# Performance work log

Hardware: AMD Instinct MI355X
Metric: run time of the kernel (lower is better)

The kernel has to match this reference:

```python
import jax, jax.numpy as jnp
import numpy as np

N, F_IN, E = 50000, 128, 800000
D1, D2, D3, NUM_LAYERS = 90, 80, 50, 4
EPS = 1e-5


def _gcn_norm(edge_index, n):
    # add self-loops, compute symmetric normalization deg^{-1/2} A_hat deg^{-1/2}
    loops = jnp.arange(n, dtype=edge_index.dtype)
    src = jnp.concatenate([edge_index[0], loops])
    dst = jnp.concatenate([edge_index[1], loops])
    deg = jax.ops.segment_sum(jnp.ones_like(src, dtype=jnp.float32), dst, num_segments=n)
    deg_isqrt = jnp.where(deg > 0, jax.lax.rsqrt(deg), 0.0)
    norm = deg_isqrt[src] * deg_isqrt[dst]  # [E+N]
    return src, dst, norm


def _gcn_conv(x, w, b, src, dst, norm, n):
    h = x @ w                                   # [N, d_out] dense transform first
    msg = h[src] * norm[:, None]                # gather + scale  [E+N, d_out]
    out = jax.ops.segment_sum(msg, dst, num_segments=n)  # scatter-add
    return out + b


def _bn(x, gamma, beta):
    # batch-statistics BatchNorm1d over node dim
    mu = jnp.mean(x, axis=0)
    var = jnp.var(x, axis=0)
    return (x - mu) * jax.lax.rsqrt(var + EPS) * gamma + beta


def setup_inputs() -> dict:
    key = jax.random.key(0)
    ks = jax.random.split(key, 16)
    s = lambda *sh: 1.0 / np.sqrt(sh[0])
    inp = {
        'x': jax.random.normal(ks[0], (N, F_IN), jnp.float32),
        'edge_index': jax.random.randint(ks[1], (2, E), 0, N, dtype=jnp.int32),
        'conv1_w': jax.random.normal(ks[2], (F_IN, D1), jnp.float32) * s(F_IN),
        'conv1_b': jnp.zeros((D1,), jnp.float32),
        'convs_w': jax.random.normal(ks[3], (NUM_LAYERS - 1, D1, D1), jnp.float32) * s(D1),
        'convs_b': jnp.zeros((NUM_LAYERS - 1, D1), jnp.float32),
        'bn1_g': jnp.ones((D1,), jnp.float32), 'bn1_b': jnp.zeros((D1,), jnp.float32),
        'fc1_w': jax.random.normal(ks[4], (D1, D2), jnp.float32) * s(D1),
        'fc1_b': jnp.zeros((D2,), jnp.float32),
        'bn2_g': jnp.ones((D2,), jnp.float32), 'bn2_b': jnp.zeros((D2,), jnp.float32),
        'fc2_w': jax.random.normal(ks[5], (D2, D3), jnp.float32) * s(D2),
        'fc2_b': jnp.zeros((D3,), jnp.float32),
        'bn3_g': jnp.ones((D3,), jnp.float32), 'bn3_b': jnp.zeros((D3,), jnp.float32),
        'fc3_w': jax.random.normal(ks[6], (D3, 1), jnp.float32) * s(D3),
        'fc3_b': jnp.zeros((1,), jnp.float32),
    }
    return inp


def reference(x, edge_index, conv1_w, conv1_b, convs_w, convs_b,
              bn1_g, bn1_b, fc1_w, fc1_b, bn2_g, bn2_b,
              fc2_w, fc2_b, bn3_g, bn3_b, fc3_w, fc3_b):
    n = x.shape[0]
    src, dst, norm = _gcn_norm(edge_index, n)
    h = jax.nn.relu(_gcn_conv(x, conv1_w, conv1_b, src, dst, norm, n))
    for i in range(convs_w.shape[0]):
        h = jax.nn.relu(_gcn_conv(h, convs_w[i], convs_b[i], src, dst, norm, n))
        h = _bn(h, bn1_g, bn1_b)
        # dropout is identity in eval mode
    h = jax.nn.relu(_bn(h @ fc1_w + fc1_b, bn2_g, bn2_b))
    h = jax.nn.relu(_bn(h @ fc2_w + fc2_b, bn3_g, bn3_b))
    return h @ fc3_w + fc3_b
```

## Files before the change

kernel.cpp:

```cpp
#include <hip/hip_runtime.h>

#define NBLK(n, b) (((n) + (b) - 1) / (b))

#define FS 96
#define FS4 24

typedef _Float16 half8_t __attribute__((ext_vector_type(8)));
typedef float float8_t __attribute__((ext_vector_type(8)));
typedef float f32x4_t __attribute__((ext_vector_type(4)));


__global__ void count_k(const int* __restrict__ dst, int* __restrict__ cnt, int e) {
  int i = blockIdx.x * blockDim.x + threadIdx.x;
  if (i < e) atomicAdd(&cnt[dst[i]], 1);
}

__global__ void isq_k(const int* __restrict__ cnt, float* __restrict__ isq, int n) {
  int i = blockIdx.x * blockDim.x + threadIdx.x;
  if (i < n) isq[i] = rsqrtf((float)cnt[i] + 1.0f);
}

__global__ __launch_bounds__(256) void scan1_k(const int* __restrict__ cnt,
                                               int* __restrict__ rowptr,
                                               int* __restrict__ partials, int n) {
  __shared__ int ls[256];
  const int t = threadIdx.x;
  const int base = blockIdx.x * 1024 + t * 4;
  int v0 = 0, v1 = 0, v2 = 0, v3 = 0;
  if (base + 3 < n) {
    int4 q = *reinterpret_cast<const int4*>(cnt + base);
    v0 = q.x; v1 = q.y; v2 = q.z; v3 = q.w;
  } else {
    if (base < n) v0 = cnt[base];
    if (base + 1 < n) v1 = cnt[base + 1];
    if (base + 2 < n) v2 = cnt[base + 2];
  }
  int s = v0 + v1 + v2 + v3;
  ls[t] = s;
  __syncthreads();
  for (int off = 1; off < 256; off <<= 1) {
    int u = (t >= off) ? ls[t - off] : 0;
    __syncthreads();
    ls[t] += u;
    __syncthreads();
  }
  int p = ls[t] - s;
  if (t == 255) partials[blockIdx.x] = ls[255];
  if (base < n) rowptr[base] = p;
  p += v0;
  if (base + 1 < n) rowptr[base + 1] = p;
  p += v1;
  if (base + 2 < n) rowptr[base + 2] = p;
  p += v2;
  if (base + 3 < n) rowptr[base + 3] = p;
}

__global__ __launch_bounds__(256) void scan2_k(const int* __restrict__ partials,
                                               int* __restrict__ offsets, int B) {
  __shared__ int ls[256];
  const int t = threadIdx.x;
  int v = (t < B) ? partials[t] : 0;
  ls[t] = v;
  __syncthreads();
  for (int off = 1; off < 256; off <<= 1) {
    int u = (t >= off) ? ls[t - off] : 0;
    __syncthreads();
    ls[t] += u;
    __syncthreads();
  }
  if (t < B) offsets[t] = ls[t] - v;
  if (t == B - 1) offsets[B] = ls[t];
}

__global__ __launch_bounds__(256) void scan3_k(int* __restrict__ rowptr,
                                               int* __restrict__ cursor,
                                               const int* __restrict__ offsets,
                                               int n, int B) {
  const int t = threadIdx.x;
  const int base = blockIdx.x * 1024 + t * 4;
  const int off = offsets[blockIdx.x];
  if (base + 3 < n) {
    int4 q = *reinterpret_cast<const int4*>(rowptr + base);
    q.x += off; q.y += off; q.z += off; q.w += off;
    *reinterpret_cast<int4*>(rowptr + base) = q;
    *reinterpret_cast<int4*>(cursor + base) = q;
  } else {
    for (int i = base; i < n; ++i) {
      int v = rowptr[i] + off;
      rowptr[i] = v;
      cursor[i] = v;
    }
  }
  if (base == 0 && blockIdx.x == 0) rowptr[n] = offsets[B];
}

__global__ __launch_bounds__(256) void fill_part_k(
    const int* __restrict__ src, const int* __restrict__ dst,
    int* __restrict__ cursor, unsigned short* __restrict__ csr, int e, int n) {
  const int p = blockIdx.x & 7;
  const int q = blockIdx.x >> 3;
  const int nb = gridDim.x >> 3;
  const int ps = (n + 7) >> 3;
  const int lo = p * ps;
  const int hi = min(lo + ps, n);
  const int stride = nb * 256;
  for (int i = q * 256 + threadIdx.x; i < e; i += stride) {
    const int d = dst[i];
    if (d >= lo && d < hi) {
      const int pos = atomicAdd(&cursor[d], 1);
      csr[pos] = (unsigned short)src[i];
    }
  }
}


template <int K, int KP, int M, int INS, int OUTS, int XF, int EPI, int NT>
__global__ __launch_bounds__(256, 2) void gemm4_k(
    const float* __restrict__ X, const float* __restrict__ W,
    const float* __restrict__ bias, const float* __restrict__ isq,
    const float* __restrict__ scale, const float* __restrict__ shift,
    void* __restrict__ OUT, int n) {
  constexpr int KG = KP / 8;
  __shared__ _Float16 Wh[NT * KG * 16 * 8];
  const int t = threadIdx.x;
  const int tbase = blockIdx.y * NT;
  for (int idx = t; idx < KP * NT * 16; idx += 256) {
    const int k = idx / (NT * 16), cl = idx - k * (NT * 16);
    const int c = tbase * 16 + cl;
    const float v = (k < K && c < M) ? W[k * M + c] : 0.0f;
    const int tt = cl >> 4, cc = cl & 15;
    Wh[((tt * KG + (k >> 3)) * 16 + cc) * 8 + (k & 7)] = (_Float16)v;
  }
  __syncthreads();
  const int wid = t >> 6;
  const int lane = t & 63;
  const int lr = lane & 15;
  const int hk = lane >> 4;
  const int r0 = blockIdx.x * 64 + wid * 16;
  const int arow = min(r0 + lr, n - 1);
  const float* __restrict__ xp = X + (size_t)arow * INS;
  const half8_t* __restrict__ Whv = reinterpret_cast<const half8_t*>(Wh);
  f32x4_t acc[NT];
#pragma unroll
  for (int tt = 0; tt < NT; ++tt) acc[tt] = (f32x4_t){0.0f, 0.0f, 0.0f, 0.0f};
  for (int ks = 0; ks < KP; ks += 32) {
    const int kb = ks + hk * 8;
    float a[8];
    {
      float4 v0 = *reinterpret_cast<const float4*>(xp + kb);
      float4 v1 = *reinterpret_cast<const float4*>(xp + kb + 4);
      a[0] = v0.x; a[1] = v0.y; a[2] = v0.z; a[3] = v0.w;
      a[4] = v1.x; a[5] = v1.y; a[6] = v1.z; a[7] = v1.w;
    }
    if constexpr (XF == 1) {
#pragma unroll
      for (int i = 0; i < 8; ++i) a[i] = fmaxf(a[i], 0.0f);
    } else if constexpr (XF == 2 || XF == 3) {
      float4 s0 = *reinterpret_cast<const float4*>(scale + kb);
      float4 s1 = *reinterpret_cast<const float4*>(scale + kb + 4);
      float4 h0 = *reinterpret_cast<const float4*>(shift + kb);
      float4 h1 = *reinterpret_cast<const float4*>(shift + kb + 4);
      const float sc[8] = {s0.x, s0.y, s0.z, s0.w, s1.x, s1.y, s1.z, s1.w};
      const float sh[8] = {h0.x, h0.y, h0.z, h0.w, h1.x, h1.y, h1.z, h1.w};
#pragma unroll
      for (int i = 0; i < 8; ++i) {
        if constexpr (XF == 2) a[i] = fmaxf(a[i], 0.0f) * sc[i] + sh[i];
        else a[i] = fmaxf(a[i] * sc[i] + sh[i], 0.0f);
      }
    }
    half8_t af;
#pragma unroll
    for (int i = 0; i < 8; ++i) af[i] = (_Float16)a[i];
    const int kg = kb >> 3;
#pragma unroll
    for (int tt = 0; tt < NT; ++tt) {
      half8_t bf = Whv[(tt * KG + kg) * 16 + lr];
      acc[tt] = __builtin_amdgcn_mfma_f32_16x16x32_f16(af, bf, acc[tt], 0, 0, 0);
    }
  }
  const int rg = r0 + (hk << 2);
  if constexpr (EPI == 0) {
    float siq[4];
#pragma unroll
    for (int j = 0; j < 4; ++j) siq[j] = (rg + j < n) ? isq[rg + j] : 0.0f;
    _Float16* Hh = (_Float16*)OUT;
#pragma unroll
    for (int tt = 0; tt < NT; ++tt) {
      const int c = (tbase + tt) * 16 + lr;
      const int tb = c / 48;
      const int so = c % 48;
#pragma unroll
      for (int j = 0; j < 4; ++j) {
        const int row = rg + j;
        if (row < n)
          Hh[(size_t)tb * n * 48 + (size_t)row * 48 + so] =
              (_Float16)(acc[tt][j] * siq[j]);
      }
    }
  } else {
    float* O = (float*)OUT;
#pragma unroll
    for (int tt = 0; tt < NT; ++tt) {
      const int c = (tbase + tt) * 16 + lr;
      const float bv = (c < M) ? bias[c] : 0.0f;
#pragma unroll
      for (int j = 0; j < 4; ++j) {
        const int row = rg + j;
        if (row < n) O[(size_t)row * OUTS + c] = acc[tt][j] + bv;
      }
    }
  }
}


template <int K, int KP, int M, int MH, int INS, int OUTS, int XF, int EPI>
__global__ __launch_bounds__(256, 2) void gemm2_k(
    const float* __restrict__ X, const float* __restrict__ W,
    const float* __restrict__ bias, const float* __restrict__ isq,
    const float* __restrict__ scale, const float* __restrict__ shift,
    void* __restrict__ OUT, int n) {
  __shared__ float Ws[KP * MH];
  __shared__ float Sc[(XF >= 2) ? KP : 1];
  __shared__ float Sh[(XF >= 2) ? KP : 1];
  const int ms = blockIdx.y;
  for (int idx = threadIdx.x; idx < KP * MH; idx += 256) {
    int k = idx / MH;
    int m = idx - k * MH;
    int col = ms * MH + m;
    Ws[idx] = (k < K && col < M) ? W[k * M + col] : 0.0f;
  }
  if constexpr (XF >= 2) {
    for (int k = threadIdx.x; k < KP; k += 256) {
      Sc[k] = (k < K) ? scale[k] : 0.0f;
      Sh[k] = (k < K) ? shift[k] : 0.0f;
    }
  }
  __syncthreads();
  const int row = blockIdx.x * 256 + threadIdx.x;
  const bool valid = row < n;
  const float* xp = X + (size_t)(valid ? row : 0) * INS;
  float acc[MH];
#pragma unroll
  for (int m = 0; m < MH; ++m) acc[m] = 0.0f;
  for (int k0 = 0; k0 < KP; k0 += 4) {
    float4 tt = *reinterpret_cast<const float4*>(xp + k0);
    float xv[4] = {tt.x, tt.y, tt.z, tt.w};
#pragma unroll
    for (int j = 0; j < 4; ++j) {
      float xval = xv[j];
      if constexpr (XF == 1) xval = fmaxf(xval, 0.0f);
      if constexpr (XF == 2) xval = fmaxf(xval, 0.0f) * Sc[k0 + j] + Sh[k0 + j];
      if constexpr (XF == 3) xval = fmaxf(xval * Sc[k0 + j] + Sh[k0 + j], 0.0f);
      const float* wrow = &Ws[(k0 + j) * MH];
#pragma unroll
      for (int m = 0; m < MH; ++m) acc[m] += xval * wrow[m];
    }
  }
  if (!valid) return;
  float* O = (float*)OUT;
  const size_t base = (size_t)row * OUTS + ms * MH;
#pragma unroll
  for (int m = 0; m < MH; ++m) O[base + m] = acc[m] + bias[ms * MH + m];
}


__global__ __launch_bounds__(256, 6) void gather_k(
    const _Float16* __restrict__ H, const int* __restrict__ rowptr,
    const unsigned short* __restrict__ csr, const float* __restrict__ isq,
    const float* __restrict__ bias, float* __restrict__ A, int n) {
  const int wid = threadIdx.x >> 6;
  const int lane = threadIdx.x & 63;
  const int d = blockIdx.x * 4 + wid;
  if (d >= n) return;
  const int g = lane >> 4;
  const int s = lane & 15;
  const int beg = rowptr[d];
  const int end = rowptr[d + 1];
  const half8_t* __restrict__ Hp = reinterpret_cast<const half8_t*>(H);
  const int sl = (s < 6) ? s : (s - 6);
  const half8_t* __restrict__ lanebase = Hp + ((s < 6) ? 0 : (size_t)n * 6) + sl;
  float8_t acc = {0, 0, 0, 0, 0, 0, 0, 0};
  float8_t acc2 = {0, 0, 0, 0, 0, 0, 0, 0};
  if (lane < 12)
    acc += __builtin_convertvector(lanebase[(size_t)d * 6], float8_t);
  int r = beg + g;
  for (; r + 4 < end; r += 8) {
    const int v0 = (int)csr[r];
    const int v1 = (int)csr[r + 4];
    if (s < 12) {
      acc += __builtin_convertvector(lanebase[(size_t)v0 * 6], float8_t);
      acc2 += __builtin_convertvector(lanebase[(size_t)v1 * 6], float8_t);
    }
  }
  for (; r < end; r += 4) {
    const int v = (int)csr[r];
    if (s < 12) acc += __builtin_convertvector(lanebase[(size_t)v * 6], float8_t);
  }
  acc += acc2;
#pragma unroll
  for (int i = 0; i < 8; ++i) acc[i] += __shfl_xor(acc[i], 16);
#pragma unroll
  for (int i = 0; i < 8; ++i) acc[i] += __shfl_xor(acc[i], 32);
  if (lane < 12) {
    const float sc = isq[d];
    const int c = lane * 8;
    float o[8];
#pragma unroll
    for (int i = 0; i < 8; ++i)
      o[i] = acc[i] * sc + ((c + i < 90) ? bias[c + i] : 0.0f);
    float4* Ap = reinterpret_cast<float4*>(A + (size_t)d * FS + c);
    Ap[0] = make_float4(o[0], o[1], o[2], o[3]);
    Ap[1] = make_float4(o[4], o[5], o[6], o[7]);
  }
}


template <int M, bool RELU>
__global__ __launch_bounds__(256) void bn_stats4_k(const float* __restrict__ X,
                                                   float* __restrict__ gsum,
                                                   float* __restrict__ gsq, int n) {
  __shared__ float ssum[FS];
  __shared__ float ssq[FS];
  for (int i = threadIdx.x; i < FS; i += 256) { ssum[i] = 0.0f; ssq[i] = 0.0f; }
  __syncthreads();
  const int t = threadIdx.x;
  const int cq = t % FS4;
  const int rl = t / FS4;
  constexpr int ROWS = 256 / FS4;
  const float4* __restrict__ Xp = reinterpret_cast<const float4*>(X);
  if (rl < ROWS) {
    float s0 = 0, s1 = 0, s2 = 0, s3 = 0, q0 = 0, q1 = 0, q2 = 0, q3 = 0;
    for (int r = blockIdx.x * ROWS + rl; r < n; r += gridDim.x * ROWS) {
      float4 v = Xp[(size_t)r * FS4 + cq];
      if (RELU) {
        v.x = fmaxf(v.x, 0.0f); v.y = fmaxf(v.y, 0.0f);
        v.z = fmaxf(v.z, 0.0f); v.w = fmaxf(v.w, 0.0f);
      }
      s0 += v.x; q0 += v.x * v.x;
      s1 += v.y; q1 += v.y * v.y;
      s2 += v.z; q2 += v.z * v.z;
      s3 += v.w; q3 += v.w * v.w;
    }
    const int c = cq * 4;
    if (c + 0 < M) { atomicAdd(&ssum[c + 0], s0); atomicAdd(&ssq[c + 0], q0); }
    if (c + 1 < M) { atomicAdd(&ssum[c + 1], s1); atomicAdd(&ssq[c + 1], q1); }
    if (c + 2 < M) { atomicAdd(&ssum[c + 2], s2); atomicAdd(&ssq[c + 2], q2); }
    if (c + 3 < M) { atomicAdd(&ssum[c + 3], s3); atomicAdd(&ssq[c + 3], q3); }
  }
  __syncthreads();
  for (int i = threadIdx.x; i < M; i += 256) {
    atomicAdd(&gsum[i], ssum[i]);
    atomicAdd(&gsq[i], ssq[i]);
  }
}


template <int M>
__global__ void bn_final_k(const float* __restrict__ gsum, const float* __restrict__ gsq,
                           const float* __restrict__ g, const float* __restrict__ b,
                           float* __restrict__ scale, float* __restrict__ shift, float invn) {
  int c = threadIdx.x;
  if (c >= FS) return;
  if (c >= M) { scale[c] = 0.0f; shift[c] = 0.0f; return; }
  float mu = gsum[c] * invn;
  float var = gsq[c] * invn - mu * mu;
  float r = rsqrtf(var + 1e-5f);
  float sc = g[c] * r;
  scale[c] = sc;
  shift[c] = b[c] - mu * sc;
}


extern "C" void kernel_launch(void* const* d_in, const int* in_sizes, int n_in,
                              void* d_out, int out_size, void* d_ws, size_t ws_size,
                              hipStream_t stream) {
  const float* x = (const float*)d_in[0];
  const int* ei = (const int*)d_in[1];
  const float* conv1_w = (const float*)d_in[2];
  const float* conv1_b = (const float*)d_in[3];
  const float* convs_w = (const float*)d_in[4];
  const float* convs_b = (const float*)d_in[5];
  const float* bn1_g = (const float*)d_in[6];
  const float* bn1_b = (const float*)d_in[7];
  const float* fc1_w = (const float*)d_in[8];
  const float* fc1_b = (const float*)d_in[9];
  const float* bn2_g = (const float*)d_in[10];
  const float* bn2_b = (const float*)d_in[11];
  const float* fc2_w = (const float*)d_in[12];
  const float* fc2_b = (const float*)d_in[13];
  const float* bn3_g = (const float*)d_in[14];
  const float* bn3_b = (const float*)d_in[15];
  const float* fc3_w = (const float*)d_in[16];
  const float* fc3_b = (const float*)d_in[17];

  const int N = in_sizes[0] / 128;
  const int E = in_sizes[1] / 2;
  const int* src = ei;
  const int* dst = ei + E;
  const int B = NBLK(N, 1024);

  float* ws = (float*)d_ws;
  float* isq = ws;
  int* rowptr = (int*)(ws + 50048);
  int* cursor = rowptr + 50048;
  int* cnt = cursor + 50048;
  unsigned short* csr16 = (unsigned short*)(cnt + 50048);
  int* partials = (int*)(csr16 + 800000);
  int* offsets = partials + 64;
  float* stats = (float*)(offsets + 128);
  float* scale = stats + 5 * 192;
  float* shift = scale + 96;
  float* bufH = shift + 96;
  float* bufA = bufH + (size_t)N * FS;
  _Float16* bufHh = (_Float16*)bufH;

  float* gs0 = stats + 0 * 192; float* gq0 = gs0 + 96;
  float* gs1 = stats + 1 * 192; float* gq1 = gs1 + 96;
  float* gs2 = stats + 2 * 192; float* gq2 = gs2 + 96;
  float* gs3 = stats + 3 * 192; float* gq3 = gs3 + 96;
  float* gs4 = stats + 4 * 192; float* gq4 = gs4 + 96;

  hipMemsetAsync(cnt, 0, 50048 * sizeof(int), stream);
  hipMemsetAsync(stats, 0, 5 * 192 * sizeof(float), stream);
  count_k<<<NBLK(E, 256), 256, 0, stream>>>(dst, cnt, E);
  isq_k<<<NBLK(N, 256), 256, 0, stream>>>(cnt, isq, N);
  scan1_k<<<B, 256, 0, stream>>>(cnt, rowptr, partials, N);
  scan2_k<<<1, 256, 0, stream>>>(partials, offsets, B);
  scan3_k<<<B, 256, 0, stream>>>(rowptr, cursor, offsets, N, B);
  fill_part_k<<<1024, 256, 0, stream>>>(src, dst, cursor, csr16, E, N);

  const int grows = NBLK(N, 256);
  const int gmf = NBLK(N, 64);
  const int ggath = NBLK(N, 4);
  const float invn = 1.0f / (float)N;

  gemm4_k<128, 128, 90, 128, FS, 0, 0, 3><<<dim3(gmf, 2), 256, 0, stream>>>(
      x, conv1_w, nullptr, isq, nullptr, nullptr, bufHh, N);
  gather_k<<<ggath, 256, 0, stream>>>(bufHh, rowptr, csr16, isq, conv1_b, bufA, N);

  gemm4_k<90, 96, 90, FS, FS, 1, 0, 3><<<dim3(gmf, 2), 256, 0, stream>>>(
      bufA, convs_w, nullptr, isq, nullptr, nullptr, bufHh, N);
  gather_k<<<ggath, 256, 0, stream>>>(bufHh, rowptr, csr16, isq, convs_b, bufA, N);
  bn_stats4_k<90, true><<<512, 256, 0, stream>>>(bufA, gs0, gq0, N);
  bn_final_k<90><<<1, 128, 0, stream>>>(gs0, gq0, bn1_g, bn1_b, scale, shift, invn);

  gemm4_k<90, 96, 90, FS, FS, 2, 0, 3><<<dim3(gmf, 2), 256, 0, stream>>>(
      bufA, convs_w + 90 * 90, nullptr, isq, scale, shift, bufHh, N);
  gather_k<<<ggath, 256, 0, stream>>>(bufHh, rowptr, csr16, isq, convs_b + 90, bufA, N);
  bn_stats4_k<90, true><<<512, 256, 0, stream>>>(bufA, gs1, gq1, N);
  bn_final_k<90><<<1, 128, 0, stream>>>(gs1, gq1, bn1_g, bn1_b, scale, shift, invn);

  gemm4_k<90, 96, 90, FS, FS, 2, 0, 3><<<dim3(gmf, 2), 256, 0, stream>>>(
      bufA, convs_w + 2 * 90 * 90, nullptr, isq, scale, shift, bufHh, N);
  gather_k<<<ggath, 256, 0, stream>>>(bufHh, rowptr, csr16, isq, convs_b + 2 * 90, bufA, N);
  bn_stats4_k<90, true><<<512, 256, 0, stream>>>(bufA, gs2, gq2, N);
  bn_final_k<90><<<1, 128, 0, stream>>>(gs2, gq2, bn1_g, bn1_b, scale, shift, invn);

  gemm4_k<90, 96, 80, FS, FS, 2, 1, 3><<<dim3(gmf, 2), 256, 0, stream>>>(
      bufA, fc1_w, fc1_b, nullptr, scale, shift, bufH, N);
  bn_stats4_k<80, false><<<512, 256, 0, stream>>>(bufH, gs3, gq3, N);
  bn_final_k<80><<<1, 128, 0, stream>>>(gs3, gq3, bn2_g, bn2_b, scale, shift, invn);

  gemm2_k<80, 80, 50, 25, FS, FS, 3, 1><<<dim3(grows, 2), 256, 0, stream>>>(
      bufH, fc2_w, fc2_b, nullptr, scale, shift, bufA, N);
  bn_stats4_k<50, false><<<512, 256, 0, stream>>>(bufA, gs4, gq4, N);
  bn_final_k<50><<<1, 128, 0, stream>>>(gs4, gq4, bn3_g, bn3_b, scale, shift, invn);

  gemm2_k<50, 52, 1, 1, FS, 1, 3, 1><<<dim3(grows, 1), 256, 0, stream>>>(
      bufA, fc3_w, fc3_b, nullptr, scale, shift, (float*)d_out, N);
}
```

Measured before the change: 476.1 us.

## Store fp16 H row-contiguous and split GEMM columns unevenly (64+32)

```diff
diff --git a/kernel.cpp b/kernel.cpp
--- a/kernel.cpp
+++ b/kernel.cpp
@@ -114,19 +114,23 @@
 }
 
 
-template <int K, int KP, int M, int INS, int OUTS, int XF, int EPI, int NT>
+template <int K, int KP, int M, int INS, int OUTS, int XF, int EPI>
 __global__ __launch_bounds__(256, 2) void gemm4_k(
     const float* __restrict__ X, const float* __restrict__ W,
     const float* __restrict__ bias, const float* __restrict__ isq,
     const float* __restrict__ scale, const float* __restrict__ shift,
     void* __restrict__ OUT, int n) {
   constexpr int KG = KP / 8;
-  __shared__ _Float16 Wh[NT * KG * 16 * 8];
+  __shared__ _Float16 Wh[4 * KG * 16 * 8];
   const int t = threadIdx.x;
-  const int tbase = blockIdx.y * NT;
-  for (int idx = t; idx < KP * NT * 16; idx += 256) {
-    const int k = idx / (NT * 16), cl = idx - k * (NT * 16);
-    const int c = tbase * 16 + cl;
+  const int ybl = blockIdx.y;
+  const int ntiles = ybl ? 2 : 4;
+  const int tbase = ybl ? 4 : 0;
+  const int nt16 = ntiles << 4;
+  const int sh = ybl ? 5 : 6;
+  for (int idx = t; idx < KP * nt16; idx += 256) {
+    const int k = idx >> sh, cl = idx & (nt16 - 1);
+    const int c = (tbase << 4) + cl;
     const float v = (k < K && c < M) ? W[k * M + c] : 0.0f;
     const int tt = cl >> 4, cc = cl & 15;
     Wh[((tt * KG + (k >> 3)) * 16 + cc) * 8 + (k & 7)] = (_Float16)v;
@@ -140,9 +144,9 @@
   const int arow = min(r0 + lr, n - 1);
   const float* __restrict__ xp = X + (size_t)arow * INS;
   const half8_t* __restrict__ Whv = reinterpret_cast<const half8_t*>(Wh);
-  f32x4_t acc[NT];
-#pragma unroll
-  for (int tt = 0; tt < NT; ++tt) acc[tt] = (f32x4_t){0.0f, 0.0f, 0.0f, 0.0f};
+  f32x4_t acc[4];
+#pragma unroll
+  for (int tt = 0; tt < 4; ++tt) acc[tt] = (f32x4_t){0.0f, 0.0f, 0.0f, 0.0f};
   for (int ks = 0; ks < KP; ks += 32) {
     const int kb = ks + hk * 8;
     float a[8];
@@ -161,11 +165,11 @@
       float4 h0 = *reinterpret_cast<const float4*>(shift + kb);
       float4 h1 = *reinterpret_cast<const float4*>(shift + kb + 4);
       const float sc[8] = {s0.x, s0.y, s0.z, s0.w, s1.x, s1.y, s1.z, s1.w};
-      const float sh[8] = {h0.x, h0.y, h0.z, h0.w, h1.x, h1.y, h1.z, h1.w};
+      const float shf[8] = {h0.x, h0.y, h0.z, h0.w, h1.x, h1.y, h1.z, h1.w};
 #pragma unroll
       for (int i = 0; i < 8; ++i) {
-        if constexpr (XF == 2) a[i] = fmaxf(a[i], 0.0f) * sc[i] + sh[i];
-        else a[i] = fmaxf(a[i] * sc[i] + sh[i], 0.0f);
+        if constexpr (XF == 2) a[i] = fmaxf(a[i], 0.0f) * sc[i] + shf[i];
+        else a[i] = fmaxf(a[i] * sc[i] + shf[i], 0.0f);
       }
     }
     half8_t af;
@@ -173,9 +177,11 @@
     for (int i = 0; i < 8; ++i) af[i] = (_Float16)a[i];
     const int kg = kb >> 3;
 #pragma unroll
-    for (int tt = 0; tt < NT; ++tt) {
-      half8_t bf = Whv[(tt * KG + kg) * 16 + lr];
-      acc[tt] = __builtin_amdgcn_mfma_f32_16x16x32_f16(af, bf, acc[tt], 0, 0, 0);
+    for (int tt = 0; tt < 4; ++tt) {
+      if (tt < ntiles) {
+        half8_t bf = Whv[(tt * KG + kg) * 16 + lr];
+        acc[tt] = __builtin_amdgcn_mfma_f32_16x16x32_f16(af, bf, acc[tt], 0, 0, 0);
+      }
     }
   }
   const int rg = r0 + (hk << 2);
@@ -185,28 +191,29 @@
     for (int j = 0; j < 4; ++j) siq[j] = (rg + j < n) ? isq[rg + j] : 0.0f;
     _Float16* Hh = (_Float16*)OUT;
 #pragma unroll
-    for (int tt = 0; tt < NT; ++tt) {
-      const int c = (tbase + tt) * 16 + lr;
-      const int tb = c / 48;
-      const int so = c % 48;
-#pragma unroll
-      for (int j = 0; j < 4; ++j) {
-        const int row = rg + j;
-        if (row < n)
-          Hh[(size_t)tb * n * 48 + (size_t)row * 48 + so] =
-              (_Float16)(acc[tt][j] * siq[j]);
+    for (int tt = 0; tt < 4; ++tt) {
+      if (tt < ntiles) {
+        const int c = (tbase + tt) * 16 + lr;
+#pragma unroll
+        for (int j = 0; j < 4; ++j) {
+          const int row = rg + j;
+          if (row < n)
+            Hh[(size_t)row * 96 + c] = (_Float16)(acc[tt][j] * siq[j]);
+        }
       }
     }
   } else {
     float* O = (float*)OUT;
 #pragma unroll
-    for (int tt = 0; tt < NT; ++tt) {
-      const int c = (tbase + tt) * 16 + lr;
-      const float bv = (c < M) ? bias[c] : 0.0f;
-#pragma unroll
-      for (int j = 0; j < 4; ++j) {
-        const int row = rg + j;
-        if (row < n) O[(size_t)row * OUTS + c] = acc[tt][j] + bv;
+    for (int tt = 0; tt < 4; ++tt) {
+      if (tt < ntiles) {
+        const int c = (tbase + tt) * 16 + lr;
+        const float bv = (c < M) ? bias[c] : 0.0f;
+#pragma unroll
+        for (int j = 0; j < 4; ++j) {
+          const int row = rg + j;
+          if (row < n) O[(size_t)row * OUTS + c] = acc[tt][j] + bv;
+        }
       }
     }
   }
@@ -277,24 +284,23 @@
   const int beg = rowptr[d];
   const int end = rowptr[d + 1];
   const half8_t* __restrict__ Hp = reinterpret_cast<const half8_t*>(H);
-  const int sl = (s < 6) ? s : (s - 6);
-  const half8_t* __restrict__ lanebase = Hp + ((s < 6) ? 0 : (size_t)n * 6) + sl;
+  const half8_t* __restrict__ lanebase = Hp + ((s < 12) ? s : 0);
   float8_t acc = {0, 0, 0, 0, 0, 0, 0, 0};
   float8_t acc2 = {0, 0, 0, 0, 0, 0, 0, 0};
   if (lane < 12)
-    acc += __builtin_convertvector(lanebase[(size_t)d * 6], float8_t);
+    acc += __builtin_convertvector(lanebase[(size_t)d * 12], float8_t);
   int r = beg + g;
   for (; r + 4 < end; r += 8) {
     const int v0 = (int)csr[r];
     const int v1 = (int)csr[r + 4];
     if (s < 12) {
-      acc += __builtin_convertvector(lanebase[(size_t)v0 * 6], float8_t);
-      acc2 += __builtin_convertvector(lanebase[(size_t)v1 * 6], float8_t);
+      acc += __builtin_convertvector(lanebase[(size_t)v0 * 12], float8_t);
+      acc2 += __builtin_convertvector(lanebase[(size_t)v1 * 12], float8_t);
     }
   }
   for (; r < end; r += 4) {
     const int v = (int)csr[r];
-    if (s < 12) acc += __builtin_convertvector(lanebase[(size_t)v * 6], float8_t);
+    if (s < 12) acc += __builtin_convertvector(lanebase[(size_t)v * 12], float8_t);
   }
   acc += acc2;
 #pragma unroll
@@ -434,29 +440,29 @@
   const int ggath = NBLK(N, 4);
   const float invn = 1.0f / (float)N;
 
-  gemm4_k<128, 128, 90, 128, FS, 0, 0, 3><<<dim3(gmf, 2), 256, 0, stream>>>(
+  gemm4_k<128, 128, 90, 128, FS, 0, 0><<<dim3(gmf, 2), 256, 0, stream>>>(
       x, conv1_w, nullptr, isq, nullptr, nullptr, bufHh, N);
   gather_k<<<ggath, 256, 0, stream>>>(bufHh, rowptr, csr16, isq, conv1_b, bufA, N);
 
-  gemm4_k<90, 96, 90, FS, FS, 1, 0, 3><<<dim3(gmf, 2), 256, 0, stream>>>(
+  gemm4_k<90, 96, 90, FS, FS, 1, 0><<<dim3(gmf, 2), 256, 0, stream>>>(
       bufA, convs_w, nullptr, isq, nullptr, nullptr, bufHh, N);
   gather_k<<<ggath, 256, 0, stream>>>(bufHh, rowptr, csr16, isq, convs_b, bufA, N);
   bn_stats4_k<90, true><<<512, 256, 0, stream>>>(bufA, gs0, gq0, N);
   bn_final_k<90><<<1, 128, 0, stream>>>(gs0, gq0, bn1_g, bn1_b, scale, shift, invn);
 
-  gemm4_k<90, 96, 90, FS, FS, 2, 0, 3><<<dim3(gmf, 2), 256, 0, stream>>>(
+  gemm4_k<90, 96, 90, FS, FS, 2, 0><<<dim3(gmf, 2), 256, 0, stream>>>(
       bufA, convs_w + 90 * 90, nullptr, isq, scale, shift, bufHh, N);
   gather_k<<<ggath, 256, 0, stream>>>(bufHh, rowptr, csr16, isq, convs_b + 90, bufA, N);
   bn_stats4_k<90, true><<<512, 256, 0, stream>>>(bufA, gs1, gq1, N);
   bn_final_k<90><<<1, 128, 0, stream>>>(gs1, gq1, bn1_g, bn1_b, scale, shift, invn);
 
-  gemm4_k<90, 96, 90, FS, FS, 2, 0, 3><<<dim3(gmf, 2), 256, 0, stream>>>(
+  gemm4_k<90, 96, 90, FS, FS, 2, 0><<<dim3(gmf, 2), 256, 0, stream>>>(
       bufA, convs_w + 2 * 90 * 90, nullptr, isq, scale, shift, bufHh, N);
   gather_k<<<ggath, 256, 0, stream>>>(bufHh, rowptr, csr16, isq, convs_b + 2 * 90, bufA, N);
   bn_stats4_k<90, true><<<512, 256, 0, stream>>>(bufA, gs2, gq2, N);
   bn_final_k<90><<<1, 128, 0, stream>>>(gs2, gq2, bn1_g, bn1_b, scale, shift, invn);
 
-  gemm4_k<90, 96, 80, FS, FS, 2, 1, 3><<<dim3(gmf, 2), 256, 0, stream>>>(
+  gemm4_k<90, 96, 80, FS, FS, 2, 1><<<dim3(gmf, 2), 256, 0, stream>>>(
       bufA, fc1_w, fc1_b, nullptr, scale, shift, bufH, N);
   bn_stats4_k<80, false><<<512, 256, 0, stream>>>(bufH, gs3, gq3, N);
   bn_final_k<80><<<1, 128, 0, stream>>>(gs3, gq3, bn2_g, bn2_b, scale, shift, invn);
```

Measured after the change: 459.1 us. 3.6% less time.
